# Performance work log

Hardware: AMD Instinct MI355X
Metric: run time of the kernel (lower is better)

## Reference

```python
import jax, jax.numpy as jnp
import numpy as np

N_HEADS = 12
NEG_INF = -1e9


def rotate_half(x):
    x1, x2 = jnp.split(x, 2, axis=-1)
    return jnp.concatenate((-x2, x1), axis=-1)


def rope_tables(T, D, dtype):
    # matches RotaryEmbedding buffers: emb = cat(freqs, freqs), shape [1,1,T,D]
    inv_freq = 1.0 / (10000.0 ** (jnp.arange(0, D, 2, dtype=jnp.float32) / D))
    t = jnp.arange(T, dtype=jnp.float32)
    freqs = jnp.einsum('i,j->ij', t, inv_freq)
    emb = jnp.concatenate((freqs, freqs), axis=-1)
    return jnp.cos(emb)[None, None].astype(dtype), jnp.sin(emb)[None, None].astype(dtype)


def setup_inputs() -> dict:
    key = jax.random.key(0)
    ks = jax.random.split(key, 5)
    B, T, C = 4, 2048, 768
    s = 1.0 / np.sqrt(C)
    x = jax.random.normal(ks[0], (B, T, C), dtype=jnp.float32)
    wq = jax.random.normal(ks[1], (C, C), dtype=jnp.float32) * s
    wk = jax.random.normal(ks[2], (C, C), dtype=jnp.float32) * s
    wv = jax.random.normal(ks[3], (C, C), dtype=jnp.float32) * s
    wo = jax.random.normal(ks[4], (C, C), dtype=jnp.float32) * s
    causal = jnp.tril(jnp.ones((T, T), dtype=bool))
    mask = jnp.where(causal, 0.0, NEG_INF).astype(jnp.float32)[None, None]
    return {"x": x, "wq": wq, "wk": wk, "wv": wv, "wo": wo, "mask": mask}


def reference(x, wq, wk, wv, wo, mask):
    B, T, C = x.shape
    H = N_HEADS
    D = C // H
    # QKV projections (no bias), reshape to [B,H,T,D]
    def proj(w):
        return (x @ w).reshape(B, T, H, D).transpose(0, 2, 1, 3)
    q, k, v = proj(wq), proj(wk), proj(wv)
    cos, sin = rope_tables(T, D, x.dtype)
    q = q * cos + rotate_half(q) * sin
    k = k * cos + rotate_half(k) * sin
    attn = jnp.einsum('bhqd,bhkd->bhqk', q, k) / jnp.sqrt(jnp.asarray(D, x.dtype))
    attn = attn + mask
    attn = jax.nn.softmax(attn, axis=-1)  # dropout = identity (eval mode)
    out = jnp.einsum('bhqk,bhkd->bhqd', attn, v)
    out = out.transpose(0, 2, 1, 3).reshape(B, T, C)
    return out @ wo
```

## Files before the change

### kernel.cpp

```cpp
#include <hip/hip_runtime.h>
#include <hip/hip_bf16.h>
#include <cmath>

typedef _Float16 f16x8 __attribute__((ext_vector_type(8)));
typedef float f32x4 __attribute__((ext_vector_type(4)));

#define T_SEQ 2048
#define C_DIM 768
#define H_NUM 12
#define NX (8192 * 768)
#define NW (768 * 768)

__device__ __forceinline__ unsigned short f2h(float f) {
    _Float16 h = (_Float16)f;
    return __builtin_bit_cast(unsigned short, h);
}

__device__ __forceinline__ float fexp2(float x) {
#if __has_builtin(__builtin_amdgcn_exp2f)
    return __builtin_amdgcn_exp2f(x);
#else
    return exp2f(x);
#endif
}

__device__ __forceinline__ unsigned int pkrtz(float a, float b) {
    auto r = __builtin_amdgcn_cvt_pkrtz(a, b);
    return __builtin_bit_cast(unsigned int, r);
}

__device__ __forceinline__ unsigned int permlo(unsigned int d0, unsigned int d1) {
#if __has_builtin(__builtin_amdgcn_perm)
    return __builtin_amdgcn_perm(d1, d0, 0x05040100u);
#else
    return (d0 & 0xffffu) | (d1 << 16);
#endif
}
__device__ __forceinline__ unsigned int permhi(unsigned int d0, unsigned int d1) {
#if __has_builtin(__builtin_amdgcn_perm)
    return __builtin_amdgcn_perm(d1, d0, 0x07060302u);
#else
    return (d0 >> 16) | (d1 & 0xffff0000u);
#endif
}

__device__ __forceinline__ void gld16(const unsigned short* g, unsigned short* l) {
    __builtin_amdgcn_global_load_lds(
        (const __attribute__((address_space(1))) unsigned int*)g,
        (__attribute__((address_space(3))) unsigned int*)l, 16, 0, 0);
}

__global__ __launch_bounds__(256)
void prep(const float* __restrict__ x,
          const float* __restrict__ w0, const float* __restrict__ w1,
          const float* __restrict__ w2, const float* __restrict__ w3,
          unsigned short* __restrict__ xb, unsigned short* __restrict__ wt) {
    __shared__ float T[64][65];
    const int pid = blockIdx.x;
    if (pid < 3072) {
        int cidx = pid * 256 + threadIdx.x;
        int row = cidx / 96;
        int cp = cidx - row * 96;
        int dchunk = row * 96 + (cp & ~3) + ((cp & 3) ^ (row & 3));
        const float* s = x + (size_t)cidx * 8;
        float4 v0 = *(const float4*)s, v1 = *(const float4*)(s + 4);
        ushort4 a, b;
        a.x = f2h(v0.x); a.y = f2h(v0.y); a.z = f2h(v0.z); a.w = f2h(v0.w);
        b.x = f2h(v1.x); b.y = f2h(v1.y); b.z = f2h(v1.z); b.w = f2h(v1.w);
        unsigned short* d = xb + (size_t)dchunk * 8;
        *(ushort4*)d = a;
        *(ushort4*)(d + 4) = b;
    } else {
        int t = pid - 3072;
        int z = t / 144, r = t - z * 144;
        int kx = r / 12, ny = r - kx * 12;
        const float* src = (z == 0) ? w0 : (z == 1) ? w1 : (z == 2) ? w2 : w3;
        unsigned short* dst = wt + (size_t)z * NW;
        const int k0 = kx * 64, n0 = ny * 64;
        const int tid = threadIdx.x;
        {
            int rowb = tid >> 4, c4 = (tid & 15) * 4;
#pragma unroll
            for (int i = 0; i < 4; ++i) {
                int row = rowb + i * 16;
                float4 v = *(const float4*)&src[(size_t)(k0 + row) * C_DIM + n0 + c4];
                T[row][c4] = v.x; T[row][c4 + 1] = v.y; T[row][c4 + 2] = v.z; T[row][c4 + 3] = v.w;
            }
        }
        __syncthreads();
        {
            int n = tid & 63, kseg = (tid >> 6) * 16;
            int n_glob = n0 + n;
            unsigned short tmp[16];
#pragma unroll
            for (int j = 0; j < 16; ++j) tmp[j] = f2h(T[kseg + j][n]);
            int base = k0 + (kseg & 32);
            int sub = (kseg >> 3) & 3;
            unsigned short* drow = dst + (size_t)n_glob * C_DIM + base;
            *(uint4*)&drow[(sub ^ (n_glob & 3)) << 3]       = *(uint4*)&tmp[0];
            *(uint4*)&drow[((sub + 1) ^ (n_glob & 3)) << 3] = *(uint4*)&tmp[8];
        }
    }
}

__global__ __launch_bounds__(256, 4)
void qkv_gemm(const unsigned short* __restrict__ xb,
              const unsigned short* __restrict__ wt,
              unsigned short* __restrict__ q_ws,
              unsigned short* __restrict__ k_ws,
              unsigned short* __restrict__ vt_ws) {
    const int pid = blockIdx.x;
    const int xcd = pid & 7, idx = pid >> 3;
    const int mloc = idx / 18, nw = idx - mloc * 18;
    const int which = nw % 3, nx = nw / 3;
    const unsigned short* W = wt + (size_t)which * NW;
    const int n0 = nx * 128, m0 = (xcd * 8 + mloc) * 128;

    __shared__ __align__(16) unsigned short As[8192];
    __shared__ __align__(16) unsigned short Bs[8192];

    const int tid = threadIdx.x, lane = tid & 63, w = tid >> 6;
    const int quad = lane >> 4, l16 = lane & 15;
    const int wm = (w >> 1) * 64, wn = (w & 1) * 64;

    f32x4 acc[4][4] = {};

    for (int k0 = 0; k0 < C_DIM; k0 += 64) {
        __syncthreads();
#pragma unroll
        for (int c = 0; c < 4; ++c) {
            int e = c * 256 + tid;
            int p = e >> 9, row = (e >> 2) & 127, ch = e & 3;
            int kc = k0 + p * 32 + ch * 8;
            gld16(xb + (size_t)(m0 + row) * C_DIM + kc, &As[e * 8]);
            gld16(W  + (size_t)(n0 + row) * C_DIM + kc, &Bs[e * 8]);
        }
        __syncthreads();
#pragma unroll
        for (int p = 0; p < 2; ++p) {
            f16x8 af[4], bf[4];
#pragma unroll
            for (int mt = 0; mt < 4; ++mt) {
                int r = wm + mt * 16 + l16;
                af[mt] = *(const f16x8*)&As[p * 4096 + r * 32 + ((quad ^ (r & 3)) << 3)];
            }
#pragma unroll
            for (int nt = 0; nt < 4; ++nt) {
                int r = wn + nt * 16 + l16;
                bf[nt] = *(const f16x8*)&Bs[p * 4096 + r * 32 + ((quad ^ (r & 3)) << 3)];
            }
#pragma unroll
            for (int mt = 0; mt < 4; ++mt)
#pragma unroll
                for (int nt = 0; nt < 4; ++nt)
                    acc[mt][nt] = __builtin_amdgcn_mfma_f32_16x16x32_f16(af[mt], bf[nt], acc[mt][nt], 0, 0, 0);
        }
    }

    const int head = nx * 2 + (w & 1);

    if (which < 2) {
        unsigned short* dst = (which == 0) ? q_ws : k_ws;
        const float qscale = 0.18033688011112042f;
#pragma unroll
        for (int ntp = 0; ntp < 2; ++ntp) {
            int d1 = ntp * 16 + l16;
            float invf = __expf(-0.28782313662425572f * (float)d1);
#pragma unroll
            for (int mt = 0; mt < 4; ++mt)
#pragma unroll
                for (int reg = 0; reg < 4; ++reg) {
                    int m = m0 + wm + mt * 16 + quad * 4 + reg;
                    int t = m & (T_SEQ - 1), bb = m >> 11;
                    float sn, cs;
                    __sincosf((float)t * invf, &sn, &cs);
                    float v1 = acc[mt][ntp][reg], v2 = acc[mt][ntp + 2][reg];
                    float o1 = v1 * cs - v2 * sn;
                    float o2 = v2 * cs + v1 * sn;
                    if (which == 0) { o1 *= qscale; o2 *= qscale; }
                    size_t o = ((size_t)(bb * H_NUM + head) * T_SEQ + t) * 64 + d1;
                    dst[o] = f2h(o1);
                    dst[o + 32] = f2h(o2);
                }
        }
    } else {
#pragma unroll
        for (int nt = 0; nt < 4; ++nt) {
            int d = nt * 16 + l16;
#pragma unroll
            for (int mt = 0; mt < 4; ++mt) {
                int m = m0 + wm + mt * 16 + quad * 4;
                int t = m & (T_SEQ - 1), bb = m >> 11;
                ushort4 pk;
                pk.x = f2h(acc[mt][nt][0]); pk.y = f2h(acc[mt][nt][1]);
                pk.z = f2h(acc[mt][nt][2]); pk.w = f2h(acc[mt][nt][3]);
                *(ushort4*)&vt_ws[((size_t)(bb * H_NUM + head) * 64 + d) * T_SEQ + t] = pk;
            }
        }
    }
}

__global__ __launch_bounds__(256, 3)
void flash_attn(const unsigned short* __restrict__ q_ws,
                const unsigned short* __restrict__ k_ws,
                const unsigned short* __restrict__ vt_ws,
                unsigned short* __restrict__ attn_out) {
    __shared__ __align__(16) unsigned short Kbuf[2][64 * 64];
    __shared__ __align__(16) unsigned short Vbuf[2][64 * 64];
    __shared__ __align__(16) unsigned int Ps32[4][16 * 64];

    const int pid = blockIdx.x;
    const int xcd = pid & 7, slot = pid >> 3;
    const int bh = xcd * 6 + (slot >> 4);
    const int pr = slot & 15;
    const int qa = pr, qb = 31 - pr;
    const int b = bh / H_NUM, h = bh % H_NUM;

    const int tid = threadIdx.x, lane = tid & 63, w = tid >> 6;
    const int quad = lane >> 4, l16 = lane & 15;
    const size_t base = (size_t)bh * (T_SEQ * 64);

    const unsigned short* qAp = q_ws + base + (size_t)(qa * 64 + w * 16 + l16) * 64 + quad * 8;
    f16x8 aqA0 = *(const f16x8*)(qAp);
    f16x8 aqA1 = *(const f16x8*)(qAp + 32);
    const unsigned short* qBp = q_ws + base + (size_t)(qb * 64 + w * 16 + l16) * 64 + quad * 8;
    f16x8 aqB0 = *(const f16x8*)(qBp);
    f16x8 aqB1 = *(const f16x8*)(qBp + 32);

    f32x4 accA[4] = {}, accB[4] = {};
    f32x4 laccA = {}, laccB = {};
    f16x8 onesf;
#pragma unroll
    for (int i = 0; i < 8; ++i) onesf[i] = (_Float16)1.0f;

    unsigned int* pw = &Ps32[w][0];

    const int r_in = lane >> 3;
    const int cpr = lane & 7;
    const int gch = (cpr ^ r_in) * 8;

#define DMA_KV(P, KT)                                                                  \
    {                                                                                  \
        _Pragma("unroll")                                                              \
        for (int j = 0; j < 2; ++j) {                                                  \
            int row = w * 16 + j * 8 + r_in;                                           \
            gld16(k_ws + base + (size_t)((KT) * 64 + row) * 64 + gch,                  \
                  &Kbuf[P][(w * 16 + j * 8) * 64]);                                    \
            gld16(vt_ws + base + (size_t)row * T_SEQ + (KT) * 64 + gch,                \
                  &Vbuf[P][(w * 16 + j * 8) * 64]);                                    \
        }                                                                              \
    }

    const int fo = (quad ^ (l16 & 7)) << 3;

    const int wg = (quad & 1) * 4;
    const int l16q = l16 >> 2, l16m = l16 & 3;
    const int s7 = l16 & 7;
    const int rA = l16 * 64;
    const int rp0a = rA + (((2 * quad) ^ s7) << 2);
    const int rp0b = rA + (((2 * quad + 1) ^ s7) << 2);

    DMA_KV(0, 0);
    for (int kt = 0; kt <= qb; ++kt) {
        const int cur = kt & 1;
        __syncthreads();
        if (kt < qb) DMA_KV(cur ^ 1, kt + 1);
        const int doA = (kt <= qa);

        f16x8 bk[4][2], bv[4][2];
#pragma unroll
        for (int nt = 0; nt < 4; ++nt) {
            const unsigned short* kr = &Kbuf[cur][(nt * 16 + l16) * 64 + fo];
            bk[nt][0] = *(const f16x8*)(kr);
            bk[nt][1] = *(const f16x8*)((const unsigned short*)((size_t)kr ^ 64));
            const unsigned short* vr = &Vbuf[cur][(nt * 16 + l16) * 64 + fo];
            bv[nt][0] = *(const f16x8*)(vr);
            bv[nt][1] = *(const f16x8*)((const unsigned short*)((size_t)vr ^ 64));
        }

        f32x4 sB[4] = {}, sA[4] = {};
#pragma unroll
        for (int nt = 0; nt < 4; ++nt) {
            sB[nt] = __builtin_amdgcn_mfma_f32_16x16x32_f16(aqB0, bk[nt][0], sB[nt], 0, 0, 0);
            sB[nt] = __builtin_amdgcn_mfma_f32_16x16x32_f16(aqB1, bk[nt][1], sB[nt], 0, 0, 0);
        }
        if (doA) {
#pragma unroll
            for (int nt = 0; nt < 4; ++nt) {
                sA[nt] = __builtin_amdgcn_mfma_f32_16x16x32_f16(aqA0, bk[nt][0], sA[nt], 0, 0, 0);
                sA[nt] = __builtin_amdgcn_mfma_f32_16x16x32_f16(aqA1, bk[nt][1], sA[nt], 0, 0, 0);
            }
        }
        if (kt == qb) {
#pragma unroll
            for (int nt = 0; nt < 4; ++nt)
#pragma unroll
                for (int reg = 0; reg < 4; ++reg)
                    if (nt * 16 + l16 > w * 16 + quad * 4 + reg) sB[nt][reg] = -1e30f;
        }
        if (kt == qa) {
#pragma unroll
            for (int nt = 0; nt < 4; ++nt)
#pragma unroll
                for (int reg = 0; reg < 4; ++reg)
                    if (nt * 16 + l16 > w * 16 + quad * 4 + reg) sA[nt][reg] = -1e30f;
        }

        if (doA) {
#pragma unroll
            for (int nt = 0; nt < 4; ++nt)
#pragma unroll
                for (int reg = 0; reg < 4; ++reg) {
                    float pB = fexp2(sB[nt][reg]);
                    float pA = fexp2(sA[nt][reg]);
                    pw[(quad * 4 + reg) * 64 + ((((nt * 4) | l16q) ^ (wg | reg)) << 2) + l16m] = pkrtz(pB, pA);
                }
        } else {
#pragma unroll
            for (int nt = 0; nt < 4; ++nt)
#pragma unroll
                for (int reg = 0; reg < 4; ++reg) {
                    float pB = fexp2(sB[nt][reg]);
                    pw[(quad * 4 + reg) * 64 + ((((nt * 4) | l16q) ^ (wg | reg)) << 2) + l16m] = pkrtz(pB, pB);
                }
        }

        uint4 c0 = *(const uint4*)(pw + rp0a);
        uint4 c1 = *(const uint4*)(pw + rp0b);
        uint4 c2 = *(const uint4*)(pw + rp0a + 32);
        uint4 c3 = *(const uint4*)(pw + rp0b + 32);

        uint4 lo0 = { permlo(c0.x, c0.y), permlo(c0.z, c0.w), permlo(c1.x, c1.y), permlo(c1.z, c1.w) };
        uint4 lo1 = { permlo(c2.x, c2.y), permlo(c2.z, c2.w), permlo(c3.x, c3.y), permlo(c3.z, c3.w) };
        f16x8 apB0 = __builtin_bit_cast(f16x8, lo0);
        f16x8 apB1 = __builtin_bit_cast(f16x8, lo1);
#pragma unroll
        for (int nt = 0; nt < 4; ++nt) {
            accB[nt] = __builtin_amdgcn_mfma_f32_16x16x32_f16(apB0, bv[nt][0], accB[nt], 0, 0, 0);
            accB[nt] = __builtin_amdgcn_mfma_f32_16x16x32_f16(apB1, bv[nt][1], accB[nt], 0, 0, 0);
        }
        laccB = __builtin_amdgcn_mfma_f32_16x16x32_f16(apB0, onesf, laccB, 0, 0, 0);
        laccB = __builtin_amdgcn_mfma_f32_16x16x32_f16(apB1, onesf, laccB, 0, 0, 0);
        if (doA) {
            uint4 hi0 = { permhi(c0.x, c0.y), permhi(c0.z, c0.w), permhi(c1.x, c1.y), permhi(c1.z, c1.w) };
            uint4 hi1 = { permhi(c2.x, c2.y), permhi(c2.z, c2.w), permhi(c3.x, c3.y), permhi(c3.z, c3.w) };
            f16x8 apA0 = __builtin_bit_cast(f16x8, hi0);
            f16x8 apA1 = __builtin_bit_cast(f16x8, hi1);
#pragma unroll
            for (int nt = 0; nt < 4; ++nt) {
                accA[nt] = __builtin_amdgcn_mfma_f32_16x16x32_f16(apA0, bv[nt][0], accA[nt], 0, 0, 0);
                accA[nt] = __builtin_amdgcn_mfma_f32_16x16x32_f16(apA1, bv[nt][1], accA[nt], 0, 0, 0);
            }
            laccA = __builtin_amdgcn_mfma_f32_16x16x32_f16(apA0, onesf, laccA, 0, 0, 0);
            laccA = __builtin_amdgcn_mfma_f32_16x16x32_f16(apA1, onesf, laccA, 0, 0, 0);
        }
    }
#undef DMA_KV

    float lB[4], lA[4];
#pragma unroll
    for (int reg = 0; reg < 4; ++reg) {
        lB[reg] = 1.0f / laccB[reg];
        lA[reg] = 1.0f / laccA[reg];
    }
#pragma unroll
    for (int nt = 0; nt < 4; ++nt)
#pragma unroll
        for (int reg = 0; reg < 4; ++reg) {
            int col = h * 64 + nt * 16 + l16;
            int tB = qb * 64 + w * 16 + quad * 4 + reg;
            attn_out[(size_t)(b * T_SEQ + tB) * C_DIM + col] = f2h(accB[nt][reg] * lB[reg]);
            int tA = qa * 64 + w * 16 + quad * 4 + reg;
            attn_out[(size_t)(b * T_SEQ + tA) * C_DIM + col] = f2h(accA[nt][reg] * lA[reg]);
        }
}

__global__ __launch_bounds__(256, 3)
void out_proj(const unsigned short* __restrict__ ab,
              const unsigned short* __restrict__ wt_o,
              float* __restrict__ out) {
    const int pid = blockIdx.x;
    const int xcd = pid & 7, idx = pid >> 3;
    const int mloc = idx / 6, nx = idx - mloc * 6;
    const int n0 = nx * 128, m0 = (xcd * 8 + mloc) * 128;

    __shared__ __align__(16) unsigned short As[8192];
    __shared__ __align__(16) unsigned short Bs[8192];

    const int tid = threadIdx.x, lane = tid & 63, w = tid >> 6;
    const int quad = lane >> 4, l16 = lane & 15;
    const int wm = (w >> 1) * 64, wn = (w & 1) * 64;

    f32x4 acc[4][4] = {};
    const int srow = tid >> 1, shalf = tid & 1;

    for (int k0 = 0; k0 < C_DIM; k0 += 64) {
        __syncthreads();
#pragma unroll
        for (int p = 0; p < 2; ++p) {
            const unsigned short* g = ab + (size_t)(m0 + srow) * C_DIM + k0 + p * 32 + shalf * 16;
            uint4 d0 = *(const uint4*)g;
            uint4 d1 = *(const uint4*)(g + 8);
            *(uint4*)&As[p * 4096 + srow * 32 + (((shalf * 2 + 0) ^ (srow & 3)) << 3)] = d0;
            *(uint4*)&As[p * 4096 + srow * 32 + (((shalf * 2 + 1) ^ (srow & 3)) << 3)] = d1;
        }
#pragma unroll
        for (int c = 0; c < 4; ++c) {
            int e = c * 256 + tid;
            int p = e >> 9, row = (e >> 2) & 127, ch = e & 3;
            gld16(wt_o + (size_t)(n0 + row) * C_DIM + k0 + p * 32 + ch * 8, &Bs[e * 8]);
        }
        __syncthreads();
#pragma unroll
        for (int p = 0; p < 2; ++p) {
            f16x8 af[4], bf[4];
#pragma unroll
            for (int mt = 0; mt < 4; ++mt) {
                int r = wm + mt * 16 + l16;
                af[mt] = *(const f16x8*)&As[p * 4096 + r * 32 + ((quad ^ (r & 3)) << 3)];
            }
#pragma unroll
            for (int nt = 0; nt < 4; ++nt) {
                int r = wn + nt * 16 + l16;
                bf[nt] = *(const f16x8*)&Bs[p * 4096 + r * 32 + ((quad ^ (r & 3)) << 3)];
            }
#pragma unroll
            for (int mt = 0; mt < 4; ++mt)
#pragma unroll
                for (int nt = 0; nt < 4; ++nt)
                    acc[mt][nt] = __builtin_amdgcn_mfma_f32_16x16x32_f16(af[mt], bf[nt], acc[mt][nt], 0, 0, 0);
        }
    }

#pragma unroll
    for (int mt = 0; mt < 4; ++mt)
#pragma unroll
        for (int nt = 0; nt < 4; ++nt)
#pragma unroll
            for (int reg = 0; reg < 4; ++reg) {
                int m = m0 + wm + mt * 16 + quad * 4 + reg;
                int n = n0 + wn + nt * 16 + l16;
                out[(size_t)m * C_DIM + n] = acc[mt][nt][reg];
            }
}

extern "C" void kernel_launch(void* const* d_in, const int* in_sizes, int n_in,
                              void* d_out, int out_size, void* d_ws, size_t ws_size,
                              hipStream_t stream) {
    const float* x  = (const float*)d_in[0];
    const float* wq = (const float*)d_in[1];
    const float* wk = (const float*)d_in[2];
    const float* wv = (const float*)d_in[3];
    const float* wo = (const float*)d_in[4];
    float* out = (float*)d_out;

    unsigned short* xb    = (unsigned short*)d_ws;
    unsigned short* wt    = xb + NX;
    unsigned short* q_ws  = wt + 4 * (size_t)NW;
    unsigned short* k_ws  = q_ws + NX;
    unsigned short* vt_ws = k_ws + NX;
    unsigned short* attn  = xb;

    prep<<<3648, 256, 0, stream>>>(x, wq, wk, wv, wo, xb, wt);
    qkv_gemm<<<1152, 256, 0, stream>>>(xb, wt, q_ws, k_ws, vt_ws);
    flash_attn<<<768, 256, 0, stream>>>(q_ws, k_ws, vt_ws, attn);
    out_proj<<<384, 256, 0, stream>>>(attn, wt + 3 * (size_t)NW, out);
}
```

Baseline: 219.8 us.

## Load V fragments directly from global, add MFMA priority hints, stagger query-tile order

Drops the shared-memory staging buffer for V and has each lane read its V^T fragments straight from global memory every iteration, which cuts LDS traffic and footprint. It wraps the MFMA blocks in s_setprio raises so compute waves get issue priority. It also rotates the query-pair assignment per head within an XCD to spread load across time. The direct global V loads are not prefetched ahead of use, so their latency may be exposed.

```diff
diff --git a/kernel.cpp b/kernel.cpp
--- a/kernel.cpp
+++ b/kernel.cpp
@@ -206,13 +206,13 @@
                 const unsigned short* __restrict__ vt_ws,
                 unsigned short* __restrict__ attn_out) {
     __shared__ __align__(16) unsigned short Kbuf[2][64 * 64];
-    __shared__ __align__(16) unsigned short Vbuf[2][64 * 64];
     __shared__ __align__(16) unsigned int Ps32[4][16 * 64];
 
     const int pid = blockIdx.x;
     const int xcd = pid & 7, slot = pid >> 3;
-    const int bh = xcd * 6 + (slot >> 4);
-    const int pr = slot & 15;
+    const int bh_l = slot >> 4;
+    const int bh = xcd * 6 + bh_l;
+    const int pr = (slot + 3 * bh_l) & 15;
     const int qa = pr, qb = 31 - pr;
     const int b = bh / H_NUM, h = bh % H_NUM;
 
@@ -239,19 +239,19 @@
     const int cpr = lane & 7;
     const int gch = (cpr ^ r_in) * 8;
 
-#define DMA_KV(P, KT)                                                                  \
+#define DMA_K(P, KT)                                                                   \
     {                                                                                  \
         _Pragma("unroll")                                                              \
         for (int j = 0; j < 2; ++j) {                                                  \
             int row = w * 16 + j * 8 + r_in;                                           \
             gld16(k_ws + base + (size_t)((KT) * 64 + row) * 64 + gch,                  \
                   &Kbuf[P][(w * 16 + j * 8) * 64]);                                    \
-            gld16(vt_ws + base + (size_t)row * T_SEQ + (KT) * 64 + gch,                \
-                  &Vbuf[P][(w * 16 + j * 8) * 64]);                                    \
         }                                                                              \
     }
 
     const int fo = (quad ^ (l16 & 7)) << 3;
+
+    const unsigned short* vrow = vt_ws + base + (size_t)l16 * T_SEQ + quad * 8;
 
     const int wg = (quad & 1) * 4;
     const int l16q = l16 >> 2, l16m = l16 & 3;
@@ -260,25 +260,31 @@
     const int rp0a = rA + (((2 * quad) ^ s7) << 2);
     const int rp0b = rA + (((2 * quad + 1) ^ s7) << 2);
 
-    DMA_KV(0, 0);
+    DMA_K(0, 0);
     for (int kt = 0; kt <= qb; ++kt) {
         const int cur = kt & 1;
         __syncthreads();
-        if (kt < qb) DMA_KV(cur ^ 1, kt + 1);
+        if (kt < qb) DMA_K(cur ^ 1, kt + 1);
         const int doA = (kt <= qa);
 
-        f16x8 bk[4][2], bv[4][2];
+        f16x8 bv[4][2];
+#pragma unroll
+        for (int nt = 0; nt < 4; ++nt) {
+            const unsigned short* vp = vrow + (size_t)nt * 16 * T_SEQ + kt * 64;
+            bv[nt][0] = *(const f16x8*)(vp);
+            bv[nt][1] = *(const f16x8*)(vp + 32);
+        }
+
+        f16x8 bk[4][2];
 #pragma unroll
         for (int nt = 0; nt < 4; ++nt) {
             const unsigned short* kr = &Kbuf[cur][(nt * 16 + l16) * 64 + fo];
             bk[nt][0] = *(const f16x8*)(kr);
             bk[nt][1] = *(const f16x8*)((const unsigned short*)((size_t)kr ^ 64));
-            const unsigned short* vr = &Vbuf[cur][(nt * 16 + l16) * 64 + fo];
-            bv[nt][0] = *(const f16x8*)(vr);
-            bv[nt][1] = *(const f16x8*)((const unsigned short*)((size_t)vr ^ 64));
         }
 
         f32x4 sB[4] = {}, sA[4] = {};
+        __builtin_amdgcn_s_setprio(1);
 #pragma unroll
         for (int nt = 0; nt < 4; ++nt) {
             sB[nt] = __builtin_amdgcn_mfma_f32_16x16x32_f16(aqB0, bk[nt][0], sB[nt], 0, 0, 0);
@@ -291,6 +297,7 @@
                 sA[nt] = __builtin_amdgcn_mfma_f32_16x16x32_f16(aqA1, bk[nt][1], sA[nt], 0, 0, 0);
             }
         }
+        __builtin_amdgcn_s_setprio(0);
         if (kt == qb) {
 #pragma unroll
             for (int nt = 0; nt < 4; ++nt)
@@ -334,6 +341,7 @@
         uint4 lo1 = { permlo(c2.x, c2.y), permlo(c2.z, c2.w), permlo(c3.x, c3.y), permlo(c3.z, c3.w) };
         f16x8 apB0 = __builtin_bit_cast(f16x8, lo0);
         f16x8 apB1 = __builtin_bit_cast(f16x8, lo1);
+        __builtin_amdgcn_s_setprio(1);
 #pragma unroll
         for (int nt = 0; nt < 4; ++nt) {
             accB[nt] = __builtin_amdgcn_mfma_f32_16x16x32_f16(apB0, bv[nt][0], accB[nt], 0, 0, 0);
@@ -341,11 +349,13 @@
         }
         laccB = __builtin_amdgcn_mfma_f32_16x16x32_f16(apB0, onesf, laccB, 0, 0, 0);
         laccB = __builtin_amdgcn_mfma_f32_16x16x32_f16(apB1, onesf, laccB, 0, 0, 0);
+        __builtin_amdgcn_s_setprio(0);
         if (doA) {
             uint4 hi0 = { permhi(c0.x, c0.y), permhi(c0.z, c0.w), permhi(c1.x, c1.y), permhi(c1.z, c1.w) };
             uint4 hi1 = { permhi(c2.x, c2.y), permhi(c2.z, c2.w), permhi(c3.x, c3.y), permhi(c3.z, c3.w) };
             f16x8 apA0 = __builtin_bit_cast(f16x8, hi0);
             f16x8 apA1 = __builtin_bit_cast(f16x8, hi1);
+            __builtin_amdgcn_s_setprio(1);
 #pragma unroll
             for (int nt = 0; nt < 4; ++nt) {
                 accA[nt] = __builtin_amdgcn_mfma_f32_16x16x32_f16(apA0, bv[nt][0], accA[nt], 0, 0, 0);
@@ -353,9 +363,10 @@
             }
             laccA = __builtin_amdgcn_mfma_f32_16x16x32_f16(apA0, onesf, laccA, 0, 0, 0);
             laccA = __builtin_amdgcn_mfma_f32_16x16x32_f16(apA1, onesf, laccA, 0, 0, 0);
-        }
-    }
-#undef DMA_KV
+            __builtin_amdgcn_s_setprio(0);
+        }
+    }
+#undef DMA_K
 
     float lB[4], lA[4];
 #pragma unroll
```

After: 256.5 us. 1.17x slower.
